# Kernel optimization log

Measured on AMD Instinct MI355X. Metric: run time of the kernel, lower is better.

The kernel has to match this reference:

```python
import jax, jax.numpy as jnp
import numpy as np
from jax import lax

K = 3  # kernel size
CO = 64  # out_channels
CI = 64  # in_channels


def setup_inputs() -> dict:
    key = jax.random.key(0)
    k1, k2, k3, k4, k5 = jax.random.split(key, 5)
    x = jax.random.normal(k1, (16, CI, 128, 128), dtype=jnp.float32)
    w1 = jax.random.normal(k2, (2 * CI, 32), dtype=jnp.float32) * 0.05
    b1 = jax.random.normal(k3, (32,), dtype=jnp.float32) * 0.05
    w2 = jax.random.normal(k4, (32, CO * CI * K * K), dtype=jnp.float32) * 0.05
    b2 = jax.random.normal(k5, (CO * CI * K * K,), dtype=jnp.float32) * 0.05
    return {"x": x, "w1": w1, "b1": b1, "w2": w2, "b2": b2}


def reference(x, w1, b1, w2, b2):
    B = x.shape[0]
    # per-sample channel statistics over spatial dims (torch.std is unbiased, ddof=1)
    mean = jnp.mean(x, axis=(2, 3))                      # [B, CI]
    std = jnp.std(x, axis=(2, 3), ddof=1)                # [B, CI]
    stats = jnp.concatenate([mean, std], axis=-1)        # [B, 2*CI]
    h = jax.nn.relu(stats @ w1 + b1)                     # [B, 32]
    kernels = (h @ w2 + b2).reshape(B, CO, CI, K, K)     # per-sample conv kernels

    def conv_one(xi, wi):
        # xi: [CI,H,W], wi: [CO,CI,K,K]; stride=1, padding=1, no bias
        return lax.conv_general_dilated(
            xi[None], wi, window_strides=(1, 1), padding=[(1, 1), (1, 1)],
            dimension_numbers=("NCHW", "OIHW", "NCHW"))[0]

    return jax.vmap(conv_one)(x, kernels)                # [B, CO, H, W]
```

## Files before the change

### kernel.cpp

```cpp
#include <hip/hip_runtime.h>
#include <hip/hip_bf16.h>


#define B_ 16
#define CI_ 64
#define CO_ 64
#define HW_ 128
#define NPIX 16384
#define KEL 36864

typedef __attribute__((ext_vector_type(4))) float f32x4;
typedef __attribute__((ext_vector_type(8))) short short8;

static __device__ __forceinline__ short bf16_of(float f) {
    __hip_bfloat16 h = __float2bfloat16(f);
    return *reinterpret_cast<short*>(&h);
}

__global__ __launch_bounds__(256) void xpose_stats(const float* __restrict__ x,
                                                   short* __restrict__ xT,
                                                   float* __restrict__ part) {
    int b = blockIdx.x, cig = blockIdx.y, pt = blockIdx.z;
    int t = threadIdx.x;
    int y = pt * 8 + (t >> 5);
    int x0 = (t & 31) * 4;

    const float* xb = x + ((size_t)(b * 64 + cig * 8)) * NPIX;
    short* xTb = xT + ((size_t)b * NPIX) * 64 + cig * 8;

    float s[8], ss[8];
    f32x4 v[8];
    #pragma unroll
    for (int c = 0; c < 8; c++) {
        v[c] = *(const f32x4*)(xb + (size_t)c * NPIX + y * 128 + x0);
        s[c]  = v[c][0] + v[c][1] + v[c][2] + v[c][3];
        ss[c] = v[c][0]*v[c][0] + v[c][1]*v[c][1] + v[c][2]*v[c][2] + v[c][3]*v[c][3];
    }
    #pragma unroll
    for (int xi = 0; xi < 4; xi++) {
        short8 o;
        #pragma unroll
        for (int c = 0; c < 8; c++) o[c] = bf16_of(v[c][xi]);
        *(short8*)(xTb + ((size_t)(y * 128 + x0 + xi)) * 64) = o;
    }

    __shared__ float red[4][16];
    int lane = t & 63, w = t >> 6;
    #pragma unroll
    for (int c = 0; c < 8; c++) {
        float a = s[c], q = ss[c];
        for (int off = 32; off; off >>= 1) { a += __shfl_down(a, off); q += __shfl_down(q, off); }
        if (lane == 0) { red[w][c * 2] = a; red[w][c * 2 + 1] = q; }
    }
    __syncthreads();
    if (t < 16)
        part[((size_t)((b * 8 + cig) * 16 + pt)) * 16 + t] =
            red[0][t] + red[1][t] + red[2][t] + red[3][t];
}

__global__ __launch_bounds__(256) void kern_gen(const float* __restrict__ part,
                                                const float* __restrict__ w1,
                                                const float* __restrict__ b1,
                                                const float* __restrict__ w2,
                                                const float* __restrict__ b2,
                                                short* __restrict__ wT) {
    int b = blockIdx.x, chunk = blockIdx.y;
    __shared__ float st[128];
    __shared__ float h[32];
    int t = threadIdx.x;
    if (t < 64) {
        int cig = t >> 3, cl = t & 7;
        const float* pb = part + ((size_t)(b * 8 + cig) * 16) * 16 + cl * 2;
        float s = 0.f, q = 0.f;
        #pragma unroll
        for (int p = 0; p < 16; p++) { s += pb[p * 16]; q += pb[p * 16 + 1]; }
        float mean = s * (1.f / NPIX);
        float var = fmaxf((q - s * mean) * (1.f / (NPIX - 1)), 0.f);
        st[t] = mean;
        st[64 + t] = sqrtf(var);
    }
    __syncthreads();
    if (t < 32) {
        float acc = b1[t];
        for (int i = 0; i < 128; i++) acc += st[i] * w1[i * 32 + t];
        h[t] = fmaxf(acc, 0.f);
    }
    __syncthreads();

    int jbase = chunk * 2304;
    float acc[9];
    #pragma unroll
    for (int tp = 0; tp < 9; tp++) acc[tp] = b2[jbase + tp * 256 + t];
    for (int i = 0; i < 32; i++) {
        float hi = h[i];
        const float* w2r = w2 + (size_t)i * KEL + jbase + t;
        #pragma unroll
        for (int tp = 0; tp < 9; tp++) acc[tp] += hi * w2r[tp * 256];
    }
    short* wb = wT + (size_t)b * 64 * 576;
    #pragma unroll
    for (int tp = 0; tp < 9; tp++) {
        int j = jbase + tp * 256 + t;
        int co = j / 576;
        int rem = j - co * 576;
        int ci = rem / 9;
        int tap = rem - ci * 9;
        wb[co * 576 + tap * 64 + ci] = bf16_of(acc[tp]);
    }
}

__global__ __launch_bounds__(512, 2) void conv_mfma(const short* __restrict__ xT,
                                                    const short* __restrict__ wT,
                                                    float* __restrict__ out) {
    __shared__ short xls[6 * 132 * 64];

    int ytile = blockIdx.x, b = blockIdx.y;
    int y0 = ytile * 4;
    int t = threadIdx.x;
    int l = t & 63, w = t >> 6;
    int ch = w & 1, r = w >> 1;
    int l15 = l & 15, lg = l >> 4;

    short8 wf[2][9][2];
    {
        const short* base = wT + ((size_t)(b * 64 + ch * 32 + l15)) * 576 + lg * 8;
        #pragma unroll
        for (int g = 0; g < 2; g++)
            #pragma unroll
            for (int tap = 0; tap < 9; tap++)
                #pragma unroll
                for (int kp = 0; kp < 2; kp++)
                    wf[g][tap][kp] = *(const short8*)(base + g * 16 * 576 + tap * 64 + kp * 32);
    }

    const short* xTb = xT + ((size_t)b) * NPIX * 64;
    for (int e = t; e < 6 * 1024; e += 512) {
        int lr = e >> 10;
        int c = e & 1023;
        int xcol = c >> 3, slot = c & 7;
        int xi = xcol + 1;
        int y = y0 - 1 + lr;
        short8 v = {0, 0, 0, 0, 0, 0, 0, 0};
        if ((unsigned)y < 128u)
            v = *(const short8*)(xTb + ((size_t)(y * 128 + xcol)) * 64 + slot * 8);
        *(short8*)(xls + (lr * 132 + xi) * 64 + ((slot ^ (xi & 7)) << 3)) = v;
    }
    if (t < 96) {
        int lr = t >> 4, cc = t & 15;
        int xi = (cc & 1) ? 129 : 0;
        int slot = cc >> 1;
        short8 z = {0, 0, 0, 0, 0, 0, 0, 0};
        *(short8*)(xls + (lr * 132 + xi) * 64 + ((slot ^ (xi & 7)) << 3)) = z;
    }
    __syncthreads();

    float* ob0 = out + ((size_t)(b * 64 + ch * 32 + lg * 4)) * NPIX + (y0 + r) * 128;
    for (int n = 0; n < 8; n++) {
        int x0 = n * 16;
        f32x4 acc0 = {0.f, 0.f, 0.f, 0.f};
        f32x4 acc1 = {0.f, 0.f, 0.f, 0.f};
        #pragma unroll
        for (int tap = 0; tap < 9; tap++) {
            const int dy = tap / 3, dx = tap % 3;
            int lr = r + dy;
            int xi = x0 + l15 + dx;
            const short* rowp = xls + (lr * 132 + xi) * 64;
            int sw = xi & 7;
            #pragma unroll
            for (int kp = 0; kp < 2; kp++) {
                short8 bfrag = *(const short8*)(rowp + (((kp * 4 + lg) ^ sw) << 3));
                acc0 = __builtin_amdgcn_mfma_f32_16x16x32_bf16(wf[0][tap][kp], bfrag, acc0, 0, 0, 0);
                acc1 = __builtin_amdgcn_mfma_f32_16x16x32_bf16(wf[1][tap][kp], bfrag, acc1, 0, 0, 0);
            }
        }
        #pragma unroll
        for (int reg = 0; reg < 4; reg++) {
            ob0[(size_t)reg * NPIX + x0 + l15] = acc0[reg];
            ob0[(size_t)(16 + reg) * NPIX + x0 + l15] = acc1[reg];
        }
    }
}

extern "C" void kernel_launch(void* const* d_in, const int* in_sizes, int n_in,
                              void* d_out, int out_size, void* d_ws, size_t ws_size,
                              hipStream_t stream) {
    const float* x  = (const float*)d_in[0];
    const float* w1 = (const float*)d_in[1];
    const float* b1 = (const float*)d_in[2];
    const float* w2 = (const float*)d_in[3];
    const float* b2 = (const float*)d_in[4];
    float* out = (float*)d_out;

    float* part = (float*)d_ws;
    short* wT = (short*)((char*)d_ws + 131072);
    short* xT = (short*)((char*)d_ws + 131072 + 1179648);

    xpose_stats<<<dim3(B_, 8, 16), 256, 0, stream>>>(x, xT, part);
    kern_gen<<<dim3(B_, 16), 256, 0, stream>>>(part, w1, b1, w2, b2, wT);
    conv_mfma<<<dim3(32, B_), 512, 0, stream>>>(xT, wT, out);
}
```

Before: 80.54 us.

## Pad transposed input, tile conv over x, batch kernel generation over samples

```diff
diff --git a/kernel.cpp b/kernel.cpp
--- a/kernel.cpp
+++ b/kernel.cpp
@@ -8,6 +8,7 @@
 #define HW_ 128
 #define NPIX 16384
 #define KEL 36864
+#define XT_RS 8320
 
 typedef __attribute__((ext_vector_type(4))) float f32x4;
 typedef __attribute__((ext_vector_type(8))) short short8;
@@ -26,7 +27,7 @@
     int x0 = (t & 31) * 4;
 
     const float* xb = x + ((size_t)(b * 64 + cig * 8)) * NPIX;
-    short* xTb = xT + ((size_t)b * NPIX) * 64 + cig * 8;
+    short* xTb = xT + (size_t)b * 128 * XT_RS;
 
     float s[8], ss[8];
     f32x4 v[8];
@@ -41,7 +42,13 @@
         short8 o;
         #pragma unroll
         for (int c = 0; c < 8; c++) o[c] = bf16_of(v[c][xi]);
-        *(short8*)(xTb + ((size_t)(y * 128 + x0 + xi)) * 64) = o;
+        *(short8*)(xTb + ((size_t)(y * 130 + x0 + xi + 1)) * 64 + cig * 8) = o;
+    }
+    if (t < 16) {
+        int y2 = pt * 8 + (t & 7);
+        int col = (t & 8) ? 129 : 0;
+        short8 z = {0, 0, 0, 0, 0, 0, 0, 0};
+        *(short8*)(xTb + ((size_t)(y2 * 130 + col)) * 64 + cig * 8) = z;
     }
 
     __shared__ float red[4][16];
@@ -64,40 +71,51 @@
                                                 const float* __restrict__ w2,
                                                 const float* __restrict__ b2,
                                                 short* __restrict__ wT) {
-    int b = blockIdx.x, chunk = blockIdx.y;
-    __shared__ float st[128];
-    __shared__ float h[32];
+    int chunk = blockIdx.x, bq = blockIdx.y;
+    __shared__ float st[16][128];
+    __shared__ float h[16][32];
     int t = threadIdx.x;
-    if (t < 64) {
-        int cig = t >> 3, cl = t & 7;
-        const float* pb = part + ((size_t)(b * 8 + cig) * 16) * 16 + cl * 2;
+
+    for (int id = t; id < 1024; id += 256) {
+        int b = id >> 6, ci = id & 63;
+        const float* pb = part + ((size_t)((b * 8 + (ci >> 3)) * 16)) * 16 + (ci & 7) * 2;
         float s = 0.f, q = 0.f;
         #pragma unroll
         for (int p = 0; p < 16; p++) { s += pb[p * 16]; q += pb[p * 16 + 1]; }
         float mean = s * (1.f / NPIX);
         float var = fmaxf((q - s * mean) * (1.f / (NPIX - 1)), 0.f);
-        st[t] = mean;
-        st[64 + t] = sqrtf(var);
-    }
-    __syncthreads();
-    if (t < 32) {
-        float acc = b1[t];
-        for (int i = 0; i < 128; i++) acc += st[i] * w1[i * 32 + t];
-        h[t] = fmaxf(acc, 0.f);
+        st[b][ci] = mean;
+        st[b][64 + ci] = sqrtf(var);
+    }
+    __syncthreads();
+    for (int id = t; id < 512; id += 256) {
+        int b = id >> 5, j = id & 31;
+        float acc = b1[j];
+        for (int i = 0; i < 128; i++) acc += st[b][i] * w1[i * 32 + j];
+        h[b][j] = fmaxf(acc, 0.f);
     }
     __syncthreads();
 
     int jbase = chunk * 2304;
-    float acc[9];
-    #pragma unroll
-    for (int tp = 0; tp < 9; tp++) acc[tp] = b2[jbase + tp * 256 + t];
+    float acc[9][4];
+    #pragma unroll
+    for (int tp = 0; tp < 9; tp++) {
+        float bv = b2[jbase + tp * 256 + t];
+        #pragma unroll
+        for (int bb = 0; bb < 4; bb++) acc[tp][bb] = bv;
+    }
     for (int i = 0; i < 32; i++) {
-        float hi = h[i];
         const float* w2r = w2 + (size_t)i * KEL + jbase + t;
-        #pragma unroll
-        for (int tp = 0; tp < 9; tp++) acc[tp] += hi * w2r[tp * 256];
-    }
-    short* wb = wT + (size_t)b * 64 * 576;
+        float hv[4];
+        #pragma unroll
+        for (int bb = 0; bb < 4; bb++) hv[bb] = h[bq * 4 + bb][i];
+        #pragma unroll
+        for (int tp = 0; tp < 9; tp++) {
+            float wv = w2r[tp * 256];
+            #pragma unroll
+            for (int bb = 0; bb < 4; bb++) acc[tp][bb] += hv[bb] * wv;
+        }
+    }
     #pragma unroll
     for (int tp = 0; tp < 9; tp++) {
         int j = jbase + tp * 256 + t;
@@ -105,79 +123,96 @@
         int rem = j - co * 576;
         int ci = rem / 9;
         int tap = rem - ci * 9;
-        wb[co * 576 + tap * 64 + ci] = bf16_of(acc[tp]);
-    }
-}
-
-__global__ __launch_bounds__(512, 2) void conv_mfma(const short* __restrict__ xT,
+        #pragma unroll
+        for (int bb = 0; bb < 4; bb++)
+            wT[(size_t)(bq * 4 + bb) * KEL + co * 576 + tap * 64 + ci] = bf16_of(acc[tp][bb]);
+    }
+}
+
+__global__ __launch_bounds__(512, 4) void conv_mfma(const short* __restrict__ xT,
                                                     const short* __restrict__ wT,
                                                     float* __restrict__ out) {
-    __shared__ short xls[6 * 132 * 64];
-
-    int ytile = blockIdx.x, b = blockIdx.y;
-    int y0 = ytile * 4;
+    __shared__ __align__(16) short xls[2][6528];
+
+    int xt = blockIdx.x, ytile = blockIdx.y, b = blockIdx.z;
+    int x0 = xt * 32, y0 = ytile * 4;
     int t = threadIdx.x;
     int l = t & 63, w = t >> 6;
     int ch = w & 1, r = w >> 1;
     int l15 = l & 15, lg = l >> 4;
 
-    short8 wf[2][9][2];
-    {
-        const short* base = wT + ((size_t)(b * 64 + ch * 32 + l15)) * 576 + lg * 8;
+    if (ytile == 0 || ytile == 31) {
+        int lr = (ytile == 0) ? 0 : 5;
+        if (t < 136) {
+            short8 z = {0, 0, 0, 0, 0, 0, 0, 0};
+            *(short8*)&xls[0][(lr * 136 + t) * 8] = z;
+            *(short8*)&xls[1][(lr * 136 + t) * 8] = z;
+        }
+    }
+
+    const short* xTb = xT + (size_t)b * 128 * XT_RS;
+    #pragma unroll
+    for (int h = 0; h < 2; h++) {
+        #pragma unroll
+        for (int it = 0; it < 2; it++) {
+            int e = it * 512 + t;
+            if (e < 816) {
+                int lr = e / 136;
+                int rem = e - lr * 136;
+                int xi = rem >> 2, q = rem & 3;
+                int y = y0 - 1 + lr;
+                if ((unsigned)y < 128u) {
+                    int o = h * 4 + (q ^ ((xi >> 1) & 3));
+                    const short* src = xTb + (size_t)y * XT_RS + (x0 + xi) * 64 + o * 8;
+                    short* dst = &xls[h][(it * 512 + (t & ~63)) * 8];
+                    __builtin_amdgcn_global_load_lds(
+                        (const __attribute__((address_space(1))) void*)src,
+                        (__attribute__((address_space(3))) void*)dst, 16, 0, 0);
+                }
+            }
+        }
+    }
+    asm volatile("s_waitcnt vmcnt(0)" ::: "memory");
+    __syncthreads();
+
+    const short* wTb = wT + ((size_t)(b * 64 + ch * 32 + l15)) * 576 + lg * 8;
+    f32x4 acc[2][2];
+    #pragma unroll
+    for (int n = 0; n < 2; n++)
+        #pragma unroll
+        for (int g = 0; g < 2; g++) acc[n][g] = (f32x4){0.f, 0.f, 0.f, 0.f};
+
+    #pragma unroll 1
+    for (int h = 0; h < 2; h++) {
+        short8 wf[2][9];
         #pragma unroll
         for (int g = 0; g < 2; g++)
             #pragma unroll
             for (int tap = 0; tap < 9; tap++)
-                #pragma unroll
-                for (int kp = 0; kp < 2; kp++)
-                    wf[g][tap][kp] = *(const short8*)(base + g * 16 * 576 + tap * 64 + kp * 32);
-    }
-
-    const short* xTb = xT + ((size_t)b) * NPIX * 64;
-    for (int e = t; e < 6 * 1024; e += 512) {
-        int lr = e >> 10;
-        int c = e & 1023;
-        int xcol = c >> 3, slot = c & 7;
-        int xi = xcol + 1;
-        int y = y0 - 1 + lr;
-        short8 v = {0, 0, 0, 0, 0, 0, 0, 0};
-        if ((unsigned)y < 128u)
-            v = *(const short8*)(xTb + ((size_t)(y * 128 + xcol)) * 64 + slot * 8);
-        *(short8*)(xls + (lr * 132 + xi) * 64 + ((slot ^ (xi & 7)) << 3)) = v;
-    }
-    if (t < 96) {
-        int lr = t >> 4, cc = t & 15;
-        int xi = (cc & 1) ? 129 : 0;
-        int slot = cc >> 1;
-        short8 z = {0, 0, 0, 0, 0, 0, 0, 0};
-        *(short8*)(xls + (lr * 132 + xi) * 64 + ((slot ^ (xi & 7)) << 3)) = z;
-    }
-    __syncthreads();
-
-    float* ob0 = out + ((size_t)(b * 64 + ch * 32 + lg * 4)) * NPIX + (y0 + r) * 128;
-    for (int n = 0; n < 8; n++) {
-        int x0 = n * 16;
-        f32x4 acc0 = {0.f, 0.f, 0.f, 0.f};
-        f32x4 acc1 = {0.f, 0.f, 0.f, 0.f};
-        #pragma unroll
-        for (int tap = 0; tap < 9; tap++) {
-            const int dy = tap / 3, dx = tap % 3;
-            int lr = r + dy;
-            int xi = x0 + l15 + dx;
-            const short* rowp = xls + (lr * 132 + xi) * 64;
-            int sw = xi & 7;
-            #pragma unroll
-            for (int kp = 0; kp < 2; kp++) {
-                short8 bfrag = *(const short8*)(rowp + (((kp * 4 + lg) ^ sw) << 3));
-                acc0 = __builtin_amdgcn_mfma_f32_16x16x32_bf16(wf[0][tap][kp], bfrag, acc0, 0, 0, 0);
-                acc1 = __builtin_amdgcn_mfma_f32_16x16x32_bf16(wf[1][tap][kp], bfrag, acc1, 0, 0, 0);
+                wf[g][tap] = *(const short8*)(wTb + g * 16 * 576 + tap * 64 + h * 32);
+        const short* xh = &xls[h][0];
+        #pragma unroll
+        for (int n = 0; n < 2; n++) {
+            #pragma unroll
+            for (int tap = 0; tap < 9; tap++) {
+                const int dy = tap / 3, dx = tap % 3;
+                int xi = n * 16 + l15 + dx;
+                short8 bf = *(const short8*)&xh[((r + dy) * 136 + xi * 4 + (lg ^ ((xi >> 1) & 3))) * 8];
+                acc[n][0] = __builtin_amdgcn_mfma_f32_16x16x32_bf16(wf[0][tap], bf, acc[n][0], 0, 0, 0);
+                acc[n][1] = __builtin_amdgcn_mfma_f32_16x16x32_bf16(wf[1][tap], bf, acc[n][1], 0, 0, 0);
             }
         }
-        #pragma unroll
-        for (int reg = 0; reg < 4; reg++) {
-            ob0[(size_t)reg * NPIX + x0 + l15] = acc0[reg];
-            ob0[(size_t)(16 + reg) * NPIX + x0 + l15] = acc1[reg];
-        }
+    }
+
+    #pragma unroll
+    for (int g = 0; g < 2; g++) {
+        float* ob = out + ((size_t)(b * 64 + ch * 32 + g * 16 + lg * 4)) * NPIX
+                        + (y0 + r) * 128 + x0 + l15;
+        #pragma unroll
+        for (int reg = 0; reg < 4; reg++)
+            #pragma unroll
+            for (int n = 0; n < 2; n++)
+                ob[(size_t)reg * NPIX + n * 16] = acc[n][g][reg];
     }
 }
 
@@ -196,6 +231,6 @@
     short* xT = (short*)((char*)d_ws + 131072 + 1179648);
 
     xpose_stats<<<dim3(B_, 8, 16), 256, 0, stream>>>(x, xT, part);
-    kern_gen<<<dim3(B_, 16), 256, 0, stream>>>(part, w1, b1, w2, b2, wT);
-    conv_mfma<<<dim3(32, B_), 512, 0, stream>>>(xT, wT, out);
-}
+    kern_gen<<<dim3(16, 4), 256, 0, stream>>>(part, w1, b1, w2, b2, wT);
+    conv_mfma<<<dim3(4, 32, B_), 512, 0, stream>>>(xT, wT, out);
+}
```

Measured after the change: 130.3 us. +61.7%, slower.
